# Kernel optimization log

Measured on AMD Instinct MI355X. Metric: run time of the kernel, lower is better.

Reference implementation:

```python
import jax, jax.numpy as jnp
import numpy as np

B, S, A, H, N = 4096, 128, 32, 1024, 256
BETA = 1.0            # params['temperature']
NORM_SMOOTHING = 0.01 # params['norm_smoothing']
MAX_A = 1.0           # env.action_space.high[0]
# dropout_rate = 0.0 and eval-mode reference -> dropout is identity


def setup_inputs() -> dict:
    key = jax.random.key(0)
    ks = jax.random.split(key, 16)
    sc_s = 1.0 / np.sqrt(S)
    sc_h = 1.0 / np.sqrt(H)
    return {
        "s": jax.random.normal(ks[0], (B, S), jnp.float32),
        "a": jax.random.normal(ks[1], (B, A), jnp.float32),
        # value side MLP: S->H->H->H->N
        "Wv1": jax.random.uniform(ks[2], (S, H), jnp.float32, -sc_s, sc_s),
        "bv1": jax.random.uniform(ks[3], (H,), jnp.float32, -sc_s, sc_s),
        "Wv2": jax.random.uniform(ks[4], (H, H), jnp.float32, -sc_h, sc_h),
        "bv2": jax.random.uniform(ks[5], (H,), jnp.float32, -sc_h, sc_h),
        "Wv3": jax.random.uniform(ks[6], (H, H), jnp.float32, -sc_h, sc_h),
        "bv3": jax.random.uniform(ks[7], (H,), jnp.float32, -sc_h, sc_h),
        "Wv4": jax.random.uniform(ks[8], (H, N), jnp.float32, -sc_h, sc_h),
        "bv4": jax.random.uniform(ks[9], (N,), jnp.float32, -sc_h, sc_h),
        # location side: S->H (xavier), then N expert linears H->A stacked
        "Wl1": jax.random.normal(ks[10], (S, H), jnp.float32) * np.sqrt(2.0 / (S + H)),
        "bl1": jnp.zeros((H,), jnp.float32),
        "Wexp": jax.random.uniform(ks[11], (N, H, A), jnp.float32, -0.1, 0.1),
        "bexp": jax.random.uniform(ks[12], (N, A), jnp.float32, -1.0, 1.0),
    }


def reference(s, a, Wv1, bv1, Wv2, bv2, Wv3, bv3, Wv4, bv4, Wl1, bl1, Wexp, bexp):
    t = jax.nn.relu(s @ Wv1 + bv1)
    t = jax.nn.relu(t @ Wv2 + bv2)
    t = jax.nn.relu(t @ Wv3 + bv3)
    values = t @ Wv4 + bv4                      # [B, N]

    # --- get_all_centroids: shared hidden, N expert heads as grouped GEMM ---
    h = jax.nn.relu(s @ Wl1 + bl1)              # [B, H] (dropout identity)
    centroids = MAX_A * jnp.tanh(
        jnp.einsum("bh,nha->bna", h, Wexp) + bexp[None]
    )                                           # [B, N, A]

    # --- rbf_function: softmax over -beta * ||centroid - a|| ---
    diff = centroids - a[:, None, :]            # [B, N, A]
    dist = jnp.sqrt(jnp.sum(diff * diff, axis=2) + NORM_SMOOTHING)  # [B, N]
    weights = jax.nn.softmax(-BETA * dist, axis=1)                  # [B, N]

    return jnp.sum(weights * values, axis=1, keepdims=True)         # [B, 1]
```

## Files before the change

### kernel.cpp

```cpp
#include <hip/hip_runtime.h>
#include <hip/hip_bf16.h>


typedef _Float16 half8 __attribute__((ext_vector_type(8)));
typedef float floatx16 __attribute__((ext_vector_type(16)));

namespace {
constexpr int kB = 4096, kS = 128, kA = 32, kH = 1024, kN = 256;
constexpr size_t al(size_t x) { return (x + 255) & ~size_t(255); }
constexpr size_t OFF_FLAG  = 0;
constexpr size_t OFF_S16   = 256;
constexpr size_t OFF_WV1T  = OFF_S16   + al((size_t)kB * kS * 2);
constexpr size_t OFF_WV2T  = OFF_WV1T  + al((size_t)kS * kH * 2);
constexpr size_t OFF_WV3T  = OFF_WV2T  + al((size_t)kH * kH * 2);
constexpr size_t OFF_WV4T  = OFF_WV3T  + al((size_t)kH * kH * 2);
constexpr size_t OFF_WL1T  = OFF_WV4T  + al((size_t)kH * kN * 2);
constexpr size_t OFF_WEXPT = OFF_WL1T  + al((size_t)kS * kH * 2);
constexpr size_t OFF_BUF1  = OFF_WEXPT + al((size_t)kN * kA * kH * 2);
constexpr size_t OFF_BUF2  = OFF_BUF1  + al((size_t)kB * kH * 2);
constexpr size_t OFF_VAL   = OFF_BUF2  + al((size_t)kB * kH * 2);
constexpr size_t OFF_DIST  = OFF_VAL   + al((size_t)kB * kN * 4);
}

__device__ __forceinline__ float ldraw(const void* p, size_t i, int bf) {
    if (bf) return __uint_as_float(((unsigned)((const unsigned short*)p)[i]) << 16);
    return ((const float*)p)[i];
}

__global__ void detect_kernel(const unsigned int* __restrict__ s_raw, int* __restrict__ flag) {
    if (threadIdx.x == 0) {
        int c = 0;
        for (int i = 0; i < 256; ++i) {
            unsigned e = (s_raw[i] >> 7) & 0xFFu;
            if (e >= 118u && e <= 135u) c++;
        }
        *flag = (c > 128) ? 1 : 0;
    }
}

__global__ void convert_to_f16(const void* __restrict__ src, _Float16* __restrict__ dst,
                               int n, const int* __restrict__ flag) {
    const int bf = *flag;
    int i = blockIdx.x * blockDim.x + threadIdx.x;
    const int stride = gridDim.x * blockDim.x;
    for (; i < n; i += stride) dst[i] = (_Float16)ldraw(src, i, bf);
}

__global__ void transpose_to_f16(const void* __restrict__ src, _Float16* __restrict__ dst,
                                 int K, int N, const int* __restrict__ flag) {
    __shared__ float tile[32][33];
    const int bf = *flag;
    const size_t zo = (size_t)blockIdx.z * K * N;
    const int n0 = blockIdx.x * 32, k0 = blockIdx.y * 32;
    const int tx = threadIdx.x, ty = threadIdx.y;
#pragma unroll
    for (int j = 0; j < 32; j += 8)
        tile[ty + j][tx] = ldraw(src, zo + (size_t)(k0 + ty + j) * N + n0 + tx, bf);
    __syncthreads();
#pragma unroll
    for (int j = 0; j < 32; j += 8)
        dst[zo + (size_t)(n0 + ty + j) * K + k0 + tx] = (_Float16)tile[tx][ty + j];
}

template <int DO_RELU, int OUT_F16>
__launch_bounds__(256)
__global__ void mfma_gemm(const _Float16* __restrict__ A, const _Float16* __restrict__ Bt,
                          const void* __restrict__ bias_raw, void* __restrict__ Cout,
                          const int* __restrict__ flagp, int N, int K) {
    __shared__ _Float16 As[2][128][16];
    __shared__ _Float16 Bs[2][128][16];
    const int tid = threadIdx.x;
    const int lane = tid & 63;
    const int w = tid >> 6, wr = w >> 1, wc = w & 1;
    const int m0 = blockIdx.y * 128, n0 = blockIdx.x * 128;

    const int r0 = tid >> 2, q = tid & 3;
    const _Float16* gA0 = A + (size_t)(m0 + r0) * K + q * 8;
    const _Float16* gA1 = gA0 + (size_t)64 * K;
    const _Float16* gB0 = Bt + (size_t)(n0 + r0) * K + q * 8;
    const _Float16* gB1 = gB0 + (size_t)64 * K;
    _Float16* lA0 = &As[q >> 1][r0][(q & 1) * 8];
    _Float16* lA1 = &As[q >> 1][r0 + 64][(q & 1) * 8];
    _Float16* lB0 = &Bs[q >> 1][r0][(q & 1) * 8];
    _Float16* lB1 = &Bs[q >> 1][r0 + 64][(q & 1) * 8];

    const int am = lane & 31;
    const int ah = (lane >> 5) * 8;
    const _Float16* pA0 = &As[0][wr * 64 + am][ah];
    const _Float16* pA1 = &As[0][wr * 64 + 32 + am][ah];
    const _Float16* pB0 = &Bs[0][wc * 64 + am][ah];
    const _Float16* pB1 = &Bs[0][wc * 64 + 32 + am][ah];

    floatx16 zero;
#pragma unroll
    for (int i = 0; i < 16; ++i) zero[i] = 0.f;
    floatx16 acc[2][2] = {zero, zero, zero, zero};

    for (int k0 = 0; k0 < K; k0 += 32) {
        float4 a0 = *(const float4*)(gA0 + k0);
        float4 a1 = *(const float4*)(gA1 + k0);
        float4 b0 = *(const float4*)(gB0 + k0);
        float4 b1 = *(const float4*)(gB1 + k0);
        __syncthreads();
        *(float4*)lA0 = a0;
        *(float4*)lA1 = a1;
        *(float4*)lB0 = b0;
        *(float4*)lB1 = b1;
        __syncthreads();
#pragma unroll
        for (int ks = 0; ks < 2; ++ks) {
            const int off = ks * (128 * 16);
            half8 af0 = *(const half8*)(pA0 + off);
            half8 af1 = *(const half8*)(pA1 + off);
            half8 bf0 = *(const half8*)(pB0 + off);
            half8 bf1 = *(const half8*)(pB1 + off);
            acc[0][0] = __builtin_amdgcn_mfma_f32_32x32x16_f16(af0, bf0, acc[0][0], 0, 0, 0);
            acc[0][1] = __builtin_amdgcn_mfma_f32_32x32x16_f16(af0, bf1, acc[0][1], 0, 0, 0);
            acc[1][0] = __builtin_amdgcn_mfma_f32_32x32x16_f16(af1, bf0, acc[1][0], 0, 0, 0);
            acc[1][1] = __builtin_amdgcn_mfma_f32_32x32x16_f16(af1, bf1, acc[1][1], 0, 0, 0);
        }
    }

    const int bf = *flagp;
    const int half = lane >> 5;
#pragma unroll
    for (int mi = 0; mi < 2; ++mi)
#pragma unroll
        for (int ni = 0; ni < 2; ++ni) {
            const int Rb = m0 + wr * 64 + mi * 32;
            const int Cb = n0 + wc * 64 + ni * 32 + am;
            const float bv = ldraw(bias_raw, Cb, bf);
#pragma unroll
            for (int rr = 0; rr < 16; ++rr) {
                const int row = Rb + (rr & 3) + 8 * (rr >> 2) + 4 * half;
                float x = acc[mi][ni][rr] + bv;
                if (DO_RELU) x = fmaxf(x, 0.f);
                if (OUT_F16) ((_Float16*)Cout)[(size_t)row * N + Cb] = (_Float16)x;
                else ((float*)Cout)[(size_t)row * N + Cb] = x;
            }
        }
}

__launch_bounds__(256)
__global__ void expert_dist_mfma(const _Float16* __restrict__ A, const _Float16* __restrict__ Bt,
                                 const void* __restrict__ bexp_raw, const void* __restrict__ a_raw,
                                 float* __restrict__ dist, const int* __restrict__ flagp) {
    constexpr int K = kH;
    __shared__ _Float16 As[2][128][16];
    __shared__ _Float16 Bs[2][128][16];
    const int tid = threadIdx.x;
    const int lane = tid & 63;
    const int w = tid >> 6, wr = w >> 1, wc = w & 1;
    const int m0 = blockIdx.y * 128, n0 = blockIdx.x * 128;

    const int r0 = tid >> 2, q = tid & 3;
    const _Float16* gA0 = A + (size_t)(m0 + r0) * K + q * 8;
    const _Float16* gA1 = gA0 + (size_t)64 * K;
    const _Float16* gB0 = Bt + (size_t)(n0 + r0) * K + q * 8;
    const _Float16* gB1 = gB0 + (size_t)64 * K;
    _Float16* lA0 = &As[q >> 1][r0][(q & 1) * 8];
    _Float16* lA1 = &As[q >> 1][r0 + 64][(q & 1) * 8];
    _Float16* lB0 = &Bs[q >> 1][r0][(q & 1) * 8];
    _Float16* lB1 = &Bs[q >> 1][r0 + 64][(q & 1) * 8];

    const int am = lane & 31;
    const int ah = (lane >> 5) * 8;
    const _Float16* pA0 = &As[0][wr * 64 + am][ah];
    const _Float16* pA1 = &As[0][wr * 64 + 32 + am][ah];
    const _Float16* pB0 = &Bs[0][wc * 64 + am][ah];
    const _Float16* pB1 = &Bs[0][wc * 64 + 32 + am][ah];

    floatx16 zero;
#pragma unroll
    for (int i = 0; i < 16; ++i) zero[i] = 0.f;
    floatx16 acc[2][2] = {zero, zero, zero, zero};

    for (int k0 = 0; k0 < K; k0 += 32) {
        float4 a0 = *(const float4*)(gA0 + k0);
        float4 a1 = *(const float4*)(gA1 + k0);
        float4 b0 = *(const float4*)(gB0 + k0);
        float4 b1 = *(const float4*)(gB1 + k0);
        __syncthreads();
        *(float4*)lA0 = a0;
        *(float4*)lA1 = a1;
        *(float4*)lB0 = b0;
        *(float4*)lB1 = b1;
        __syncthreads();
#pragma unroll
        for (int ks = 0; ks < 2; ++ks) {
            const int off = ks * (128 * 16);
            half8 af0 = *(const half8*)(pA0 + off);
            half8 af1 = *(const half8*)(pA1 + off);
            half8 bf0 = *(const half8*)(pB0 + off);
            half8 bf1 = *(const half8*)(pB1 + off);
            acc[0][0] = __builtin_amdgcn_mfma_f32_32x32x16_f16(af0, bf0, acc[0][0], 0, 0, 0);
            acc[0][1] = __builtin_amdgcn_mfma_f32_32x32x16_f16(af0, bf1, acc[0][1], 0, 0, 0);
            acc[1][0] = __builtin_amdgcn_mfma_f32_32x32x16_f16(af1, bf0, acc[1][0], 0, 0, 0);
            acc[1][1] = __builtin_amdgcn_mfma_f32_32x32x16_f16(af1, bf1, acc[1][1], 0, 0, 0);
        }
    }

    __syncthreads();
    float* red = (float*)&As[0][0][0];
    const int bf = *flagp;
    const int half = lane >> 5;

#pragma unroll
    for (int mi = 0; mi < 2; ++mi) {
        const int Rb = m0 + wr * 64 + mi * 32;
        float av[16];
#pragma unroll
        for (int rr = 0; rr < 16; ++rr) {
            const int row = Rb + (rr & 3) + 8 * (rr >> 2) + 4 * half;
            av[rr] = ldraw(a_raw, (size_t)row * kA + am, bf);
        }
#pragma unroll
        for (int ni = 0; ni < 2; ++ni) {
            const int Cb = n0 + wc * 64 + ni * 32;
            const int e = Cb >> 5;
            const float be = ldraw(bexp_raw, Cb + am, bf);
            float s[16];
#pragma unroll
            for (int rr = 0; rr < 16; ++rr) {
                const float c = tanhf(acc[mi][ni][rr] + be);
                const float d = c - av[rr];
                s[rr] = d * d;
            }
#pragma unroll
            for (int msk = 1; msk <= 16; msk <<= 1)
#pragma unroll
                for (int rr = 0; rr < 16; ++rr)
                    s[rr] += __shfl_xor(s[rr], msk, 64);
            if (am == 0) {
#pragma unroll
                for (int rr = 0; rr < 16; ++rr) red[w * 32 + half * 16 + rr] = s[rr];
            }
            if (am < 16) {
                const float ss = red[w * 32 + half * 16 + am];
                const int row = Rb + (am & 3) + 8 * (am >> 2) + 4 * half;
                dist[(size_t)row * kN + e] = sqrtf(ss + 0.01f);
            }
        }
    }
}

__launch_bounds__(256)
__global__ void final_kernel(const float* __restrict__ dist, const float* __restrict__ values,
                             const int* __restrict__ flag, void* __restrict__ out) {
    const int b = blockIdx.x;
    const int n = threadIdx.x;
    const float d = dist[(size_t)b * kN + n];
    const float v = values[(size_t)b * kN + n];
    const int wid = n >> 6, lane = n & 63;
    __shared__ float red[8];
    __shared__ float rw[4], rwv[4];

    float m = d;
    for (int off = 32; off > 0; off >>= 1) m = fminf(m, __shfl_down(m, off));
    if (lane == 0) red[wid] = m;
    __syncthreads();
    if (n == 0) red[4] = fminf(fminf(red[0], red[1]), fminf(red[2], red[3]));
    __syncthreads();
    const float dmin = red[4];

    float wgt = expf(dmin - d);
    float wv = wgt * v;
    for (int off = 32; off > 0; off >>= 1) {
        wgt += __shfl_down(wgt, off);
        wv += __shfl_down(wv, off);
    }
    if (lane == 0) { rw[wid] = wgt; rwv[wid] = wv; }
    __syncthreads();
    if (n == 0) {
        const float sw = rw[0] + rw[1] + rw[2] + rw[3];
        const float swv = rwv[0] + rwv[1] + rwv[2] + rwv[3];
        const float o = swv / sw;
        if (*flag) ((__hip_bfloat16*)out)[b] = __float2bfloat16(o);
        else       ((float*)out)[b] = o;
    }
}

extern "C" void kernel_launch(void* const* d_in, const int* in_sizes, int n_in,
                              void* d_out, int out_size, void* d_ws, size_t ws_size,
                              hipStream_t stream) {
    (void)in_sizes; (void)n_in; (void)out_size; (void)ws_size;
    char* ws = (char*)d_ws;
    int* flag = (int*)(ws + OFF_FLAG);
    _Float16* s16   = (_Float16*)(ws + OFF_S16);
    _Float16* wv1t  = (_Float16*)(ws + OFF_WV1T);
    _Float16* wv2t  = (_Float16*)(ws + OFF_WV2T);
    _Float16* wv3t  = (_Float16*)(ws + OFF_WV3T);
    _Float16* wv4t  = (_Float16*)(ws + OFF_WV4T);
    _Float16* wl1t  = (_Float16*)(ws + OFF_WL1T);
    _Float16* wexpt = (_Float16*)(ws + OFF_WEXPT);
    _Float16* buf1  = (_Float16*)(ws + OFF_BUF1);
    _Float16* buf2  = (_Float16*)(ws + OFF_BUF2);
    float* values   = (float*)(ws + OFF_VAL);
    float* dist     = (float*)(ws + OFF_DIST);

    detect_kernel<<<1, 64, 0, stream>>>((const unsigned int*)d_in[0], flag);
    convert_to_f16<<<512, 256, 0, stream>>>(d_in[0], s16, kB * kS, flag);

    dim3 tb(32, 8);
    transpose_to_f16<<<dim3(kH / 32, kS / 32, 1), tb, 0, stream>>>(d_in[2],  wv1t,  kS, kH, flag);
    transpose_to_f16<<<dim3(kH / 32, kH / 32, 1), tb, 0, stream>>>(d_in[4],  wv2t,  kH, kH, flag);
    transpose_to_f16<<<dim3(kH / 32, kH / 32, 1), tb, 0, stream>>>(d_in[6],  wv3t,  kH, kH, flag);
    transpose_to_f16<<<dim3(kN / 32, kH / 32, 1), tb, 0, stream>>>(d_in[8],  wv4t,  kH, kN, flag);
    transpose_to_f16<<<dim3(kH / 32, kS / 32, 1), tb, 0, stream>>>(d_in[10], wl1t,  kS, kH, flag);
    transpose_to_f16<<<dim3(kA / 32, kH / 32, kN), tb, 0, stream>>>(d_in[12], wexpt, kH, kA, flag);

    mfma_gemm<1, 1><<<dim3(kH / 128, kB / 128), 256, 0, stream>>>(s16,  wv1t, d_in[3], buf1, flag, kH, kS);
    mfma_gemm<1, 1><<<dim3(kH / 128, kB / 128), 256, 0, stream>>>(buf1, wv2t, d_in[5], buf2, flag, kH, kH);
    mfma_gemm<1, 1><<<dim3(kH / 128, kB / 128), 256, 0, stream>>>(buf2, wv3t, d_in[7], buf1, flag, kH, kH);
    mfma_gemm<0, 0><<<dim3(kN / 128, kB / 128), 256, 0, stream>>>(buf1, wv4t, d_in[9], values, flag, kN, kH);
    mfma_gemm<1, 1><<<dim3(kH / 128, kB / 128), 256, 0, stream>>>(s16,  wl1t, d_in[11], buf2, flag, kH, kS);

    expert_dist_mfma<<<dim3((kN * kA) / 128, kB / 128), 256, 0, stream>>>(
        buf2, wexpt, d_in[13], d_in[1], dist, flag);

    final_kernel<<<kB, 256, 0, stream>>>(dist, values, flag, d_out);
}
```

Measured before the change: 368.9 us.

## Use direct global-to-LDS loads in GEMM and split expert distance epilogue

The MFMA GEMM now stages A/B tiles with global_load_lds, which writes directly into shared memory without passing through registers. It also uses a K-step of 64 with a new LDS layout. The expert GEMM reuses the generic GEMM to write the pre-tanh fp16 logits z (B x N*A) to the workspace, placed over the dead weight buffers. A fused final kernel then computes fast tanh, the distance to a, the softmax and the weighted sum. This removes the shuffle-heavy reduction epilogue, but adds a 64MB fp16 intermediate write and read, and fp16 rounding of the logits before tanh.

```diff
diff --git a/kernel.cpp b/kernel.cpp
--- a/kernel.cpp
+++ b/kernel.cpp
@@ -10,21 +10,33 @@
 constexpr size_t al(size_t x) { return (x + 255) & ~size_t(255); }
 constexpr size_t OFF_FLAG  = 0;
 constexpr size_t OFF_S16   = 256;
-constexpr size_t OFF_WV1T  = OFF_S16   + al((size_t)kB * kS * 2);
+constexpr size_t OFF_WEXPT = OFF_S16   + al((size_t)kB * kS * 2);
+constexpr size_t OFF_BUF2  = OFF_WEXPT + al((size_t)kN * kA * kH * 2);
+constexpr size_t OFF_VAL   = OFF_BUF2  + al((size_t)kB * kH * 2);
+constexpr size_t OFF_WV1T  = OFF_VAL   + al((size_t)kB * kN * 4);
 constexpr size_t OFF_WV2T  = OFF_WV1T  + al((size_t)kS * kH * 2);
 constexpr size_t OFF_WV3T  = OFF_WV2T  + al((size_t)kH * kH * 2);
 constexpr size_t OFF_WV4T  = OFF_WV3T  + al((size_t)kH * kH * 2);
 constexpr size_t OFF_WL1T  = OFF_WV4T  + al((size_t)kH * kN * 2);
-constexpr size_t OFF_WEXPT = OFF_WL1T  + al((size_t)kS * kH * 2);
-constexpr size_t OFF_BUF1  = OFF_WEXPT + al((size_t)kN * kA * kH * 2);
-constexpr size_t OFF_BUF2  = OFF_BUF1  + al((size_t)kB * kH * 2);
-constexpr size_t OFF_VAL   = OFF_BUF2  + al((size_t)kB * kH * 2);
-constexpr size_t OFF_DIST  = OFF_VAL   + al((size_t)kB * kN * 4);
+constexpr size_t OFF_BUF1  = OFF_WL1T  + al((size_t)kS * kH * 2);
+constexpr size_t OFF_Z     = OFF_WV1T;
 }
 
 __device__ __forceinline__ float ldraw(const void* p, size_t i, int bf) {
     if (bf) return __uint_as_float(((unsigned)((const unsigned short*)p)[i]) << 16);
     return ((const float*)p)[i];
+}
+
+__device__ __forceinline__ void gl_lds16(const void* g, void* l) {
+    __builtin_amdgcn_global_load_lds(
+        (const __attribute__((address_space(1))) unsigned int*)g,
+        (__attribute__((address_space(3))) unsigned int*)l, 16, 0, 0);
+}
+
+__device__ __forceinline__ float fast_tanh(float x) {
+    x = fminf(9.f, fmaxf(-9.f, x));
+    float e = __expf(2.f * x);
+    return (e - 1.f) * __builtin_amdgcn_rcpf(e + 1.f);
 }
 
 __global__ void detect_kernel(const unsigned int* __restrict__ s_raw, int* __restrict__ flag) {
@@ -67,61 +79,49 @@
 __global__ void mfma_gemm(const _Float16* __restrict__ A, const _Float16* __restrict__ Bt,
                           const void* __restrict__ bias_raw, void* __restrict__ Cout,
                           const int* __restrict__ flagp, int N, int K) {
-    __shared__ _Float16 As[2][128][16];
-    __shared__ _Float16 Bs[2][128][16];
+    __shared__ _Float16 As[8192];
+    __shared__ _Float16 Bs[8192];
     const int tid = threadIdx.x;
     const int lane = tid & 63;
     const int w = tid >> 6, wr = w >> 1, wc = w & 1;
     const int m0 = blockIdx.y * 128, n0 = blockIdx.x * 128;
 
-    const int r0 = tid >> 2, q = tid & 3;
-    const _Float16* gA0 = A + (size_t)(m0 + r0) * K + q * 8;
-    const _Float16* gA1 = gA0 + (size_t)64 * K;
-    const _Float16* gB0 = Bt + (size_t)(n0 + r0) * K + q * 8;
-    const _Float16* gB1 = gB0 + (size_t)64 * K;
-    _Float16* lA0 = &As[q >> 1][r0][(q & 1) * 8];
-    _Float16* lA1 = &As[q >> 1][r0 + 64][(q & 1) * 8];
-    _Float16* lB0 = &Bs[q >> 1][r0][(q & 1) * 8];
-    _Float16* lB1 = &Bs[q >> 1][r0 + 64][(q & 1) * 8];
-
-    const int am = lane & 31;
-    const int ah = (lane >> 5) * 8;
-    const _Float16* pA0 = &As[0][wr * 64 + am][ah];
-    const _Float16* pA1 = &As[0][wr * 64 + 32 + am][ah];
-    const _Float16* pB0 = &Bs[0][wc * 64 + am][ah];
-    const _Float16* pB1 = &Bs[0][wc * 64 + 32 + am][ah];
+    const _Float16* gA = A + (size_t)(m0 + w * 32 + (lane & 31)) * K + (lane >> 5) * 8;
+    const _Float16* gB = Bt + (size_t)(n0 + w * 32 + (lane & 31)) * K + (lane >> 5) * 8;
+    _Float16* lA = As + (size_t)(w * 64 + lane) * 8;
+    _Float16* lB = Bs + (size_t)(w * 64 + lane) * 8;
+
+    const _Float16* pA = As + (size_t)(wr * 2 * 64 + lane) * 8;
+    const _Float16* pB = Bs + (size_t)(wc * 2 * 64 + lane) * 8;
 
     floatx16 zero;
 #pragma unroll
     for (int i = 0; i < 16; ++i) zero[i] = 0.f;
     floatx16 acc[2][2] = {zero, zero, zero, zero};
 
-    for (int k0 = 0; k0 < K; k0 += 32) {
-        float4 a0 = *(const float4*)(gA0 + k0);
-        float4 a1 = *(const float4*)(gA1 + k0);
-        float4 b0 = *(const float4*)(gB0 + k0);
-        float4 b1 = *(const float4*)(gB1 + k0);
+    for (int k0 = 0; k0 < K; k0 += 64) {
+#pragma unroll
+        for (int t = 0; t < 4; ++t) {
+            gl_lds16(gA + k0 + t * 16, lA + t * 2048);
+            gl_lds16(gB + k0 + t * 16, lB + t * 2048);
+        }
         __syncthreads();
-        *(float4*)lA0 = a0;
-        *(float4*)lA1 = a1;
-        *(float4*)lB0 = b0;
-        *(float4*)lB1 = b1;
-        __syncthreads();
-#pragma unroll
-        for (int ks = 0; ks < 2; ++ks) {
-            const int off = ks * (128 * 16);
-            half8 af0 = *(const half8*)(pA0 + off);
-            half8 af1 = *(const half8*)(pA1 + off);
-            half8 bf0 = *(const half8*)(pB0 + off);
-            half8 bf1 = *(const half8*)(pB1 + off);
+#pragma unroll
+        for (int ks = 0; ks < 4; ++ks) {
+            half8 af0 = *(const half8*)(pA + ks * 2048);
+            half8 af1 = *(const half8*)(pA + ks * 2048 + 512);
+            half8 bf0 = *(const half8*)(pB + ks * 2048);
+            half8 bf1 = *(const half8*)(pB + ks * 2048 + 512);
             acc[0][0] = __builtin_amdgcn_mfma_f32_32x32x16_f16(af0, bf0, acc[0][0], 0, 0, 0);
             acc[0][1] = __builtin_amdgcn_mfma_f32_32x32x16_f16(af0, bf1, acc[0][1], 0, 0, 0);
             acc[1][0] = __builtin_amdgcn_mfma_f32_32x32x16_f16(af1, bf0, acc[1][0], 0, 0, 0);
             acc[1][1] = __builtin_amdgcn_mfma_f32_32x32x16_f16(af1, bf1, acc[1][1], 0, 0, 0);
         }
+        __syncthreads();
     }
 
     const int bf = *flagp;
+    const int am = lane & 31;
     const int half = lane >> 5;
 #pragma unroll
     for (int mi = 0; mi < 2; ++mi)
@@ -142,120 +142,38 @@
 }
 
 __launch_bounds__(256)
-__global__ void expert_dist_mfma(const _Float16* __restrict__ A, const _Float16* __restrict__ Bt,
-                                 const void* __restrict__ bexp_raw, const void* __restrict__ a_raw,
-                                 float* __restrict__ dist, const int* __restrict__ flagp) {
-    constexpr int K = kH;
-    __shared__ _Float16 As[2][128][16];
-    __shared__ _Float16 Bs[2][128][16];
-    const int tid = threadIdx.x;
-    const int lane = tid & 63;
-    const int w = tid >> 6, wr = w >> 1, wc = w & 1;
-    const int m0 = blockIdx.y * 128, n0 = blockIdx.x * 128;
-
-    const int r0 = tid >> 2, q = tid & 3;
-    const _Float16* gA0 = A + (size_t)(m0 + r0) * K + q * 8;
-    const _Float16* gA1 = gA0 + (size_t)64 * K;
-    const _Float16* gB0 = Bt + (size_t)(n0 + r0) * K + q * 8;
-    const _Float16* gB1 = gB0 + (size_t)64 * K;
-    _Float16* lA0 = &As[q >> 1][r0][(q & 1) * 8];
-    _Float16* lA1 = &As[q >> 1][r0 + 64][(q & 1) * 8];
-    _Float16* lB0 = &Bs[q >> 1][r0][(q & 1) * 8];
-    _Float16* lB1 = &Bs[q >> 1][r0 + 64][(q & 1) * 8];
-
-    const int am = lane & 31;
-    const int ah = (lane >> 5) * 8;
-    const _Float16* pA0 = &As[0][wr * 64 + am][ah];
-    const _Float16* pA1 = &As[0][wr * 64 + 32 + am][ah];
-    const _Float16* pB0 = &Bs[0][wc * 64 + am][ah];
-    const _Float16* pB1 = &Bs[0][wc * 64 + 32 + am][ah];
-
-    floatx16 zero;
-#pragma unroll
-    for (int i = 0; i < 16; ++i) zero[i] = 0.f;
-    floatx16 acc[2][2] = {zero, zero, zero, zero};
-
-    for (int k0 = 0; k0 < K; k0 += 32) {
-        float4 a0 = *(const float4*)(gA0 + k0);
-        float4 a1 = *(const float4*)(gA1 + k0);
-        float4 b0 = *(const float4*)(gB0 + k0);
-        float4 b1 = *(const float4*)(gB1 + k0);
-        __syncthreads();
-        *(float4*)lA0 = a0;
-        *(float4*)lA1 = a1;
-        *(float4*)lB0 = b0;
-        *(float4*)lB1 = b1;
-        __syncthreads();
-#pragma unroll
-        for (int ks = 0; ks < 2; ++ks) {
-            const int off = ks * (128 * 16);
-            half8 af0 = *(const half8*)(pA0 + off);
-            half8 af1 = *(const half8*)(pA1 + off);
-            half8 bf0 = *(const half8*)(pB0 + off);
-            half8 bf1 = *(const half8*)(pB1 + off);
-            acc[0][0] = __builtin_amdgcn_mfma_f32_32x32x16_f16(af0, bf0, acc[0][0], 0, 0, 0);
-            acc[0][1] = __builtin_amdgcn_mfma_f32_32x32x16_f16(af0, bf1, acc[0][1], 0, 0, 0);
-            acc[1][0] = __builtin_amdgcn_mfma_f32_32x32x16_f16(af1, bf0, acc[1][0], 0, 0, 0);
-            acc[1][1] = __builtin_amdgcn_mfma_f32_32x32x16_f16(af1, bf1, acc[1][1], 0, 0, 0);
-        }
-    }
-
-    __syncthreads();
-    float* red = (float*)&As[0][0][0];
-    const int bf = *flagp;
-    const int half = lane >> 5;
-
-#pragma unroll
-    for (int mi = 0; mi < 2; ++mi) {
-        const int Rb = m0 + wr * 64 + mi * 32;
-        float av[16];
-#pragma unroll
-        for (int rr = 0; rr < 16; ++rr) {
-            const int row = Rb + (rr & 3) + 8 * (rr >> 2) + 4 * half;
-            av[rr] = ldraw(a_raw, (size_t)row * kA + am, bf);
-        }
-#pragma unroll
-        for (int ni = 0; ni < 2; ++ni) {
-            const int Cb = n0 + wc * 64 + ni * 32;
-            const int e = Cb >> 5;
-            const float be = ldraw(bexp_raw, Cb + am, bf);
-            float s[16];
-#pragma unroll
-            for (int rr = 0; rr < 16; ++rr) {
-                const float c = tanhf(acc[mi][ni][rr] + be);
-                const float d = c - av[rr];
-                s[rr] = d * d;
-            }
-#pragma unroll
-            for (int msk = 1; msk <= 16; msk <<= 1)
-#pragma unroll
-                for (int rr = 0; rr < 16; ++rr)
-                    s[rr] += __shfl_xor(s[rr], msk, 64);
-            if (am == 0) {
-#pragma unroll
-                for (int rr = 0; rr < 16; ++rr) red[w * 32 + half * 16 + rr] = s[rr];
-            }
-            if (am < 16) {
-                const float ss = red[w * 32 + half * 16 + am];
-                const int row = Rb + (am & 3) + 8 * (am >> 2) + 4 * half;
-                dist[(size_t)row * kN + e] = sqrtf(ss + 0.01f);
-            }
-        }
-    }
-}
-
-__launch_bounds__(256)
-__global__ void final_kernel(const float* __restrict__ dist, const float* __restrict__ values,
-                             const int* __restrict__ flag, void* __restrict__ out) {
+__global__ void final_fused(const _Float16* __restrict__ z, const void* __restrict__ a_raw,
+                            const float* __restrict__ values, const int* __restrict__ flag,
+                            void* __restrict__ out) {
     const int b = blockIdx.x;
     const int n = threadIdx.x;
-    const float d = dist[(size_t)b * kN + n];
+    const int bf = *flag;
+    __shared__ float as_[32];
+    if (n < 32) as_[n] = ldraw(a_raw, (size_t)b * kA + n, bf);
+    __syncthreads();
+
+    const _Float16* zp = z + (size_t)b * (kN * kA) + n * kA;
+    float zl[32];
+#pragma unroll
+    for (int t = 0; t < 4; ++t) {
+        half8 h = *(const half8*)(zp + t * 8);
+#pragma unroll
+        for (int j = 0; j < 8; ++j) zl[t * 8 + j] = (float)h[j];
+    }
+    float sum = 0.f;
+#pragma unroll
+    for (int a = 0; a < 32; ++a) {
+        const float c = fast_tanh(zl[a]);
+        const float d = c - as_[a];
+        sum = fmaf(d, d, sum);
+    }
+    const float dist = sqrtf(sum + 0.01f);
     const float v = values[(size_t)b * kN + n];
+
     const int wid = n >> 6, lane = n & 63;
     __shared__ float red[8];
     __shared__ float rw[4], rwv[4];
-
-    float m = d;
+    float m = dist;
     for (int off = 32; off > 0; off >>= 1) m = fminf(m, __shfl_down(m, off));
     if (lane == 0) red[wid] = m;
     __syncthreads();
@@ -263,7 +181,7 @@
     __syncthreads();
     const float dmin = red[4];
 
-    float wgt = expf(dmin - d);
+    float wgt = expf(dmin - dist);
     float wv = wgt * v;
     for (int off = 32; off > 0; off >>= 1) {
         wgt += __shfl_down(wgt, off);
@@ -275,8 +193,8 @@
         const float sw = rw[0] + rw[1] + rw[2] + rw[3];
         const float swv = rwv[0] + rwv[1] + rwv[2] + rwv[3];
         const float o = swv / sw;
-        if (*flag) ((__hip_bfloat16*)out)[b] = __float2bfloat16(o);
-        else       ((float*)out)[b] = o;
+        if (bf) ((__hip_bfloat16*)out)[b] = __float2bfloat16(o);
+        else    ((float*)out)[b] = o;
     }
 }
 
@@ -296,7 +214,7 @@
     _Float16* buf1  = (_Float16*)(ws + OFF_BUF1);
     _Float16* buf2  = (_Float16*)(ws + OFF_BUF2);
     float* values   = (float*)(ws + OFF_VAL);
-    float* dist     = (float*)(ws + OFF_DIST);
+    _Float16* z     = (_Float16*)(ws + OFF_Z);
 
     detect_kernel<<<1, 64, 0, stream>>>((const unsigned int*)d_in[0], flag);
     convert_to_f16<<<512, 256, 0, stream>>>(d_in[0], s16, kB * kS, flag);
@@ -314,9 +232,6 @@
     mfma_gemm<1, 1><<<dim3(kH / 128, kB / 128), 256, 0, stream>>>(buf2, wv3t, d_in[7], buf1, flag, kH, kH);
     mfma_gemm<0, 0><<<dim3(kN / 128, kB / 128), 256, 0, stream>>>(buf1, wv4t, d_in[9], values, flag, kN, kH);
     mfma_gemm<1, 1><<<dim3(kH / 128, kB / 128), 256, 0, stream>>>(s16,  wl1t, d_in[11], buf2, flag, kH, kS);
-
-    expert_dist_mfma<<<dim3((kN * kA) / 128, kB / 128), 256, 0, stream>>>(
-        buf2, wexpt, d_in[13], d_in[1], dist, flag);
-
-    final_kernel<<<kB, 256, 0, stream>>>(dist, values, flag, d_out);
-}
+    mfma_gemm<0, 1><<<dim3((kN * kA) / 128, kB / 128), 256, 0, stream>>>(buf2, wexpt, d_in[13], z, flag, kN * kA, kH);
+    final_fused<<<kB, 256, 0, stream>>>(z, d_in[1], values, flag, d_out);
+}
```

After: 393.9 us. 6.8% more time.
